# Optimization experiments

Measured on AMD Instinct MI355X. Metric: run time of the kernel, lower is better.

Reference implementation:

```python
import jax, jax.numpy as jnp
import numpy as np

ANG = 5   # angular resolution (u = v = 5, n = 25 views)
CH = 64   # input channels
D = 2 * CH  # spa_dim + ang_dim + fre_dim = c/2 + c/2 + c = 128
NEG = -1e15


def _l2(x):
    # torch F.normalize over the contraction axis (last axis of folded layout)
    n = jnp.sqrt(jnp.sum(x * x, axis=-1, keepdims=True))
    return x / jnp.maximum(n, 1e-12)


def setup_inputs() -> dict:
    key = jax.random.key(0)
    ks = jax.random.split(key, 8)
    b, c, n, h, w = 4, CH, ANG * ANG, 32, 32
    d = D
    return {
        "x_lf": jax.random.normal(ks[0], (b, c, n, h, w), jnp.float32),
        "x_hf": jax.random.normal(ks[1], (b, c, n, h, w), jnp.float32),
        "W_in": jax.random.normal(ks[2], (c, d), jnp.float32) / np.sqrt(c).astype(np.float32),
        "W_kv": jax.random.normal(ks[3], (c, d), jnp.float32) / np.sqrt(c).astype(np.float32),
        "ln_g": jnp.ones((d,), jnp.float32),
        "ln_b": jnp.zeros((d,), jnp.float32),
        "W_m1": jax.random.normal(ks[4], (d, d), jnp.float32) / np.sqrt(d).astype(np.float32),
        "W_m2": jax.random.normal(ks[5], (d, d), jnp.float32) / np.sqrt(d).astype(np.float32),
        "W_out": jax.random.normal(ks[6], (d, c), jnp.float32) / np.sqrt(d).astype(np.float32),
    }


def _attend(fold, unfold, tq, tk, tv):
    # fold(t): (b, cc, u*v, h, w) -> (b, M, K); k/v use the same folding
    qf = _l2(fold(tq))            # q normalized over contraction axis
    kf = _l2(fold(tk))            # k normalized over contraction axis (dim=-2 of k^T)
    vf = fold(tv)
    att = jnp.einsum('bmk,bnk->bmn', qf, kf)   # (b, M, M)
    M = att.shape[-1]
    tril = jnp.tril(jnp.ones((M, M), bool))    # causal mask over folded axis
    att = jax.nn.softmax(jnp.where(tril, att, NEG), axis=-1)
    return unfold(att @ vf) + tv               # residual with token_v


def reference(x_lf, x_hf, W_in, W_kv, ln_g, ln_b, W_m1, W_m2, W_out):
    b, c, n, h, w = x_hf.shape
    u = v = ANG
    d = W_in.shape[1]

    def to_tokens(x, W):
        # 'b c (u v) h w -> (b u v) (h w) c' ; Linear ; back to 'b d (u v) h w'
        xt = x.reshape(b, c, u, v, h, w).transpose(0, 2, 3, 4, 5, 1).reshape(b * u * v, h * w, c)
        y = xt @ W
        return y.reshape(b, u, v, h, w, d).transpose(0, 5, 1, 2, 3, 4).reshape(b, d, u * v, h, w)

    q = to_tokens(x_hf, W_in)
    kv = to_tokens(x_lf, W_kv)
    cq = d // 4
    sf_q, af_q, sa_q = q[:, :cq], q[:, cq:2 * cq], q[:, 2 * cq:]
    sf_kv, af_kv, sa_kv = kv[:, :cq], kv[:, cq:2 * cq], kv[:, 2 * cq:]

    # SpatialFrequency: 'b c (u v) h w -> b (c h) (w u v)'
    def sf_fold(t):
        cc = t.shape[1]
        return t.reshape(b, cc, u, v, h, w).transpose(0, 1, 4, 5, 2, 3).reshape(b, cc * h, w * u * v)
    def sf_unfold(t):
        cc = t.shape[1] // h
        return t.reshape(b, cc, h, w, u, v).transpose(0, 1, 4, 5, 2, 3).reshape(b, cc, u * v, h, w)

    # AngularFrequency: 'b c (u v) h w -> b (c u) (h v w)'
    def af_fold(t):
        cc = t.shape[1]
        return t.reshape(b, cc, u, v, h, w).transpose(0, 1, 2, 4, 3, 5).reshape(b, cc * u, h * v * w)
    def af_unfold(t):
        cc = t.shape[1] // u
        return t.reshape(b, cc, u, h, v, w).transpose(0, 1, 2, 4, 3, 5).reshape(b, cc, u * v, h, w)

    # SpatialAngular: 'b c (u v) h w -> b (h u) (c v w)'
    def sa_fold(t):
        cc = t.shape[1]
        return t.reshape(b, cc, u, v, h, w).transpose(0, 4, 2, 1, 3, 5).reshape(b, h * u, cc * v * w)
    def sa_unfold(t):
        cc = t.shape[2] // (v * w) if t.ndim == 3 else t.shape[1]
        t = t.reshape(b, h, u, cc, v, w)
        return t.transpose(0, 3, 2, 4, 1, 5).reshape(b, cc, u * v, h, w)

    sf = _attend(sf_fold, sf_unfold, sf_q, sf_kv, sf_kv)
    af = _attend(af_fold, af_unfold, af_q, af_kv, af_kv)
    sa = _attend(sa_fold, sa_unfold, sa_q, sa_kv, sa_kv)

    cat = jnp.concatenate([sf, af, sa], axis=1)  # (b, d, n, h, w)
    ct = cat.reshape(b, d, u, v, h, w).transpose(0, 2, 3, 4, 5, 1).reshape(b * u * v, h * w, d)

    # c_mlp: LayerNorm -> Linear -> ReLU -> Linear (dropout is identity in eval)
    mu = jnp.mean(ct, axis=-1, keepdims=True)
    var = jnp.mean(jnp.square(ct - mu), axis=-1, keepdims=True)
    ln = (ct - mu) / jnp.sqrt(var + 1e-5) * ln_g + ln_b
    mlp = jax.nn.relu(ln @ W_m1) @ W_m2
    out_t = (mlp + ct) @ W_out  # residual then output projection

    out = out_t.reshape(b, u, v, h, w, -1).transpose(0, 5, 1, 2, 3, 4).reshape(b, -1, u * v, h, w)
    return out
```

## Files before the change

kernel.cpp:

```cpp
#include <hip/hip_runtime.h>

#define NSP   25600
#define HWC   1024

typedef __attribute__((ext_vector_type(8))) short bf8;
typedef __attribute__((ext_vector_type(4))) float f4;
#define MFMA(a,b,c) __builtin_amdgcn_mfma_f32_16x16x32_bf16(a, b, c, 0, 0, 0)
typedef unsigned short u16;

__device__ __forceinline__ u16 f2b(float f) {
    union { float f; unsigned u; } v; v.f = f;
    unsigned r = v.u + 0x7fffu + ((v.u >> 16) & 1u);
    return (u16)(r >> 16);
}
__device__ __forceinline__ float b2f(u16 h) {
    union { unsigned u; float f; } v; v.u = ((unsigned)h) << 16;
    return v.f;
}

__device__ __forceinline__ long row_base(int att, int b, int m) {
    if (att == 0) { int cc = m >> 5, h = m & 31;   return ((long)(b*128 + cc))*NSP + h*32; }
    else if (att == 1) { int cc = m / 5, u = m - cc*5; return ((long)(b*128 + 32 + cc))*NSP + u*5120; }
    else { int h = m / 5, u = m - h*5;            return ((long)(b*128 + 64))*NSP + u*5120 + h*32; }
}
__device__ __forceinline__ long chunk_off(int att, int kc) {
    if (att == 0) return (long)kc * 1024;
    else if (att == 1) return (long)kc * 32;
    else { int cc = kc / 5, v = kc - cc*5; return (long)cc*NSP + v*1024; }
}

__global__ __launch_bounds__(256) void k_prep(
        const float* __restrict__ Wi, const float* __restrict__ Wk,
        const float* __restrict__ W1, const float* __restrict__ W2,
        const float* __restrict__ Wo, u16* __restrict__ wbt) {
    int e = blockIdx.x * 256 + threadIdx.x;
    const float* src; int base, K, N;
    if (e < 8192)       { src = Wi; base = 0;     K = 64;  N = 128; }
    else if (e < 16384) { src = Wk; base = 8192;  K = 64;  N = 128; }
    else if (e < 32768) { src = W1; base = 16384; K = 128; N = 128; }
    else if (e < 49152) { src = W2; base = 32768; K = 128; N = 128; }
    else                { src = Wo; base = 49152; K = 128; N = 64;  }
    int local = e - base, n = local / K, k = local - n * K;
    wbt[e] = f2b(src[k * N + n]);
}

__global__ __launch_bounds__(256) void k_tokens(
        const float* __restrict__ x_hf, const float* __restrict__ x_lf,
        const u16* __restrict__ wbt,
        u16* __restrict__ qb, u16* __restrict__ kvb) {
    int s0 = blockIdx.x * 64, b = blockIdx.y, which = blockIdx.z;
    const float* x  = which ? x_lf : x_hf;
    const u16* Wb = wbt + (which ? 8192 : 0);
    u16* out = which ? kvb : qb;
    __shared__ u16 Axs[64 * 72];
    __shared__ u16 Wl [128 * 72];
    int tid = threadIdx.x;
    for (int g = tid; g < 1024; g += 256) {
        int d = g >> 3, c8 = (g & 7) * 8;
        *(bf8*)&Wl[d * 72 + c8] = *(const bf8*)(Wb + d * 64 + c8);
    }
    for (int g = tid; g < 1024; g += 256) {
        int s = g & 63, c4 = (g >> 6) * 4;
        long xb = ((long)(b * 64 + c4)) * NSP + s0 + s;
        ushort4 pk;
        pk.x = f2b(x[xb]);
        pk.y = f2b(x[xb + NSP]);
        pk.z = f2b(x[xb + 2 * NSP]);
        pk.w = f2b(x[xb + 3 * NSP]);
        *(ushort4*)&Axs[s * 72 + c4] = pk;
    }
    __syncthreads();
    int w = tid >> 6, l = tid & 63, quad = l >> 4, col = l & 15;
    f4 z = {0.f, 0.f, 0.f, 0.f};
    f4 acc[8]; for (int i = 0; i < 8; ++i) acc[i] = z;
#pragma unroll
    for (int kc = 0; kc < 2; ++kc) {
        bf8 a = *(bf8*)&Axs[(w * 16 + col) * 72 + kc * 32 + quad * 8];
#pragma unroll
        for (int nt = 0; nt < 8; ++nt) {
            bf8 bb = *(bf8*)&Wl[(nt * 16 + col) * 72 + kc * 32 + quad * 8];
            acc[nt] = MFMA(a, bb, acc[nt]);
        }
    }
#pragma unroll
    for (int nt = 0; nt < 8; ++nt) {
        int d = nt * 16 + col;
        long base = ((long)(b * 128 + d)) * NSP + s0 + w * 16 + quad * 4;
        ushort4 pk;
        pk.x = f2b(acc[nt][0]); pk.y = f2b(acc[nt][1]);
        pk.z = f2b(acc[nt][2]); pk.w = f2b(acc[nt][3]);
        *(ushort4*)(out + base) = pk;
    }
}

__global__ __launch_bounds__(256) void k_vt_norms(
        const u16* __restrict__ qb, const u16* __restrict__ kvb,
        u16* __restrict__ vt0, u16* __restrict__ vt1, u16* __restrict__ vt2,
        float* __restrict__ nq, float* __restrict__ nk) {
    int x = blockIdx.x, b = blockIdx.y;
    int tid = threadIdx.x;
    if (x < 3200) {
        int att, kc, pt, P, KC; u16* vt;
        if (x < 800)       { att = 0; kc = x >> 5; pt = (x & 31) * 32; P = 1024; KC = 25;  vt = vt0; }
        else if (x < 1600) { int x2 = x - 800;  att = 1; kc = x2 / 5; pt = (x2 - kc * 5) * 32; P = 160; KC = 160; vt = vt1; }
        else               { int x3 = x - 1600; att = 2; kc = x3 / 5; pt = (x3 - kc * 5) * 32; P = 160; KC = 320; vt = vt2; }
        long co = chunk_off(att, kc);
        __shared__ u16 T[32 * 36];
        {
            int r = tid >> 3, fq = (tid & 7) * 4;
            ushort4 e = *(const ushort4*)(kvb + row_base(att, b, pt + r) + co + fq);
            *(ushort4*)&T[r * 36 + fq] = e;
        }
        __syncthreads();
        {
            int f = tid >> 3, p4 = (tid & 7) * 4;
            ushort4 pk;
            pk.x = T[(p4    ) * 36 + f];
            pk.y = T[(p4 + 1) * 36 + f];
            pk.z = T[(p4 + 2) * 36 + f];
            pk.w = T[(p4 + 3) * 36 + f];
            *(ushort4*)(vt + ((long)b * KC + kc) * 32 * P + (long)f * P + pt + p4) = pk;
        }
    } else {
        int x2 = x - 3200;
        int which = x2 >= 336;
        int g = which ? x2 - 336 : x2;
        int att, m0, KC;
        if (g < 256)      { att = 0; m0 = g * 4;         KC = 25;  }
        else if (g < 296) { att = 1; m0 = (g - 256) * 4; KC = 160; }
        else              { att = 2; m0 = (g - 296) * 4; KC = 320; }
        const u16* src = which ? kvb : qb;
        float* dst = which ? nk : nq;
        int w = tid >> 6, lane = tid & 63;
        int m = m0 + w;
        long base = row_base(att, b, m);
        int K = KC * 32;
        float s = 0.f;
        for (int k8 = lane * 8; k8 < K; k8 += 512) {
            bf8 v = *(const bf8*)(src + base + chunk_off(att, k8 >> 5) + (k8 & 31));
#pragma unroll
            for (int j = 0; j < 8; ++j) { float f = b2f(((u16*)&v)[j]); s += f * f; }
        }
        for (int o = 32; o >= 1; o >>= 1) s += __shfl_xor(s, o);
        if (lane == 0) {
            int off = (att == 0) ? b * 1024 + m
                                 : ((att == 1) ? 4096 : 4736) + b * 160 + m;
            dst[off] = fmaxf(sqrtf(s), 1e-12f);
        }
    }
}

__global__ __launch_bounds__(256) void k_sgemm_all(
        const u16* __restrict__ qb, const u16* __restrict__ kvb,
        const float* __restrict__ nq, const float* __restrict__ nk,
        u16* __restrict__ Sb, float* __restrict__ Spart) {
    __shared__ float lds[4096];
    int x = blockIdx.x, b = blockIdx.y;
    int tid = threadIdx.x, w = tid >> 6, l = tid & 63, quad = l >> 4, col = l & 15;
    if (x < 136) {
        u16* Qs = (u16*)lds;
        u16* Ks = Qs + 64 * 40;
        int t = x, i = 0;
        while (t >= (i + 1) * (i + 2) / 2) ++i;
        int j = t - i * (i + 1) / 2;
        int mt = i * 64, nt = j * 64;
        int srow = tid >> 2, g = tid & 3;
        f4 z = {0.f, 0.f, 0.f, 0.f};
        f4 acc[4]; for (int q = 0; q < 4; ++q) acc[q] = z;
        for (int kc = 0; kc < 25; ++kc) {
            long co = (long)kc * 1024;
            {
                int m = mt + srow;
                *(bf8*)&Qs[srow * 40 + g * 8] =
                    *(const bf8*)(qb + ((long)(b*128 + (m >> 5)))*NSP + (m & 31)*32 + co + g*8);
                int n = nt + srow;
                *(bf8*)&Ks[srow * 40 + g * 8] =
                    *(const bf8*)(kvb + ((long)(b*128 + (n >> 5)))*NSP + (n & 31)*32 + co + g*8);
            }
            __syncthreads();
            bf8 a = *(bf8*)&Qs[(w * 16 + col) * 40 + quad * 8];
#pragma unroll
            for (int t2 = 0; t2 < 4; ++t2) {
                bf8 bb = *(bf8*)&Ks[(t2 * 16 + col) * 40 + quad * 8];
                acc[t2] = MFMA(a, bb, acc[t2]);
            }
            __syncthreads();
        }
#pragma unroll
        for (int t2 = 0; t2 < 4; ++t2)
#pragma unroll
            for (int r = 0; r < 4; ++r) {
                int m = mt + w * 16 + quad * 4 + r, n = nt + t2 * 16 + col;
                float v = (n <= m) ? acc[t2][r] / (nq[b*1024 + m] * nk[b*1024 + n]) : 0.f;
                Sb[((long)b * 1024 + m) * 1024 + n] = f2b(v);
            }
    } else {
        int x2 = x - 136;
        int t = x2 % 15, y = x2 / 15;
        int att, split, nsplit; float* base;
        if (y < 10) { att = 1; split = y;      nsplit = 10; base = Spart; }
        else        { att = 2; split = y - 10; nsplit = 20; base = Spart + 614400; }
        int i = 0;
        while (t >= (i + 1) * (i + 2) / 2) ++i;
        int j = t - i * (i + 1) / 2;
        int mt = i * 32, nt = j * 32;
        long rm0 = row_base(att, b, mt + col),      rm1 = row_base(att, b, mt + 16 + col);
        long rn0 = row_base(att, b, nt + col),      rn1 = row_base(att, b, nt + 16 + col);
        int ko = quad * 8;
        f4 z = {0.f, 0.f, 0.f, 0.f};
        f4 a00 = z, a01 = z, a10 = z, a11 = z;
#pragma unroll
        for (int s = 0; s < 4; ++s) {
            int kc = split * 16 + w * 4 + s;
            long co = chunk_off(att, kc);
            bf8 qa0 = *(const bf8*)(qb + rm0 + co + ko);
            bf8 qa1 = *(const bf8*)(qb + rm1 + co + ko);
            bf8 kb0 = *(const bf8*)(kvb + rn0 + co + ko);
            bf8 kb1 = *(const bf8*)(kvb + rn1 + co + ko);
            a00 = MFMA(qa0, kb0, a00); a01 = MFMA(qa0, kb1, a01);
            a10 = MFMA(qa1, kb0, a10); a11 = MFMA(qa1, kb1, a11);
        }
        float* my = lds + w * 1024;
#pragma unroll
        for (int r = 0; r < 4; ++r) {
            my[(quad * 4 + r) * 32 + col]            = a00[r];
            my[(quad * 4 + r) * 32 + 16 + col]       = a01[r];
            my[(16 + quad * 4 + r) * 32 + col]       = a10[r];
            my[(16 + quad * 4 + r) * 32 + 16 + col]  = a11[r];
        }
        __syncthreads();
        float* dst = base + ((long)((b * 15 + t) * nsplit + split)) * 1024;
        for (int e = tid; e < 1024; e += 256)
            dst[e] = lds[e] + lds[1024 + e] + lds[2048 + e] + lds[3072 + e];
    }
}

__global__ __launch_bounds__(256) void k_softmax_all(
        const u16* __restrict__ Sb, u16* __restrict__ Pb,
        const float* __restrict__ Spart, const float* __restrict__ nq,
        const float* __restrict__ nk, u16* __restrict__ Pb12) {
    int xb = blockIdx.x, b = blockIdx.y, tid = threadIdx.x;
    if (xb < 256) {
        int w = tid >> 6, lane = tid & 63;
        int m = xb * 4 + w;
        const u16* row = Sb + ((long)b * 1024 + m) * 1024;
        u16* pr = Pb + ((long)b * 1024 + m) * 1024;
        int e0 = lane * 16;
        bf8 x0 = *(const bf8*)(row + e0);
        bf8 x1 = *(const bf8*)(row + e0 + 8);
        float v[16];
#pragma unroll
        for (int j = 0; j < 8; ++j) { v[j] = b2f(((u16*)&x0)[j]); v[8 + j] = b2f(((u16*)&x1)[j]); }
        float mx = -1e30f;
#pragma unroll
        for (int j = 0; j < 16; ++j) if (e0 + j <= m) mx = fmaxf(mx, v[j]);
#pragma unroll
        for (int o = 32; o >= 1; o >>= 1) mx = fmaxf(mx, __shfl_xor(mx, o));
        float s = 0.f;
#pragma unroll
        for (int j = 0; j < 16; ++j) {
            float e = (e0 + j <= m) ? __expf(v[j] - mx) : 0.f;
            v[j] = e; s += e;
        }
#pragma unroll
        for (int o = 32; o >= 1; o >>= 1) s += __shfl_xor(s, o);
        float inv = 1.f / s;
        bf8 o0, o1;
#pragma unroll
        for (int j = 0; j < 8; ++j) {
            ((u16*)&o0)[j] = f2b(v[j] * inv);
            ((u16*)&o1)[j] = f2b(v[8 + j] * inv);
        }
        *(bf8*)(pr + e0) = o0;
        *(bf8*)(pr + e0 + 8) = o1;
    } else {
        int x = xb - 256;
        int att = (x < 160) ? 1 : 2;
        int m = (att == 1) ? x : x - 160;
        int nsplit = (att == 1) ? 10 : 20;
        const float* base = (att == 1) ? Spart : Spart + 614400;
        int noff = (att == 1) ? 4096 : 4736;
        u16* P = Pb12 + ((att == 1) ? 0 : 102400);
        int i = m >> 5, ro = (m & 31) * 32;
        int n = tid;
        bool act = (n <= m) && (n < 160);
        float myv = 0.f;
        if (act) {
            int t = i * (i + 1) / 2 + (n >> 5);
            const float* src = base + ((long)((b * 15 + t) * nsplit)) * 1024 + ro + (n & 31);
            float s = 0.f;
            for (int sp = 0; sp < nsplit; ++sp) s += src[(long)sp * 1024];
            myv = s / (nq[noff + b * 160 + m] * nk[noff + b * 160 + n]);
        }
        __shared__ float red[256];
        red[tid] = act ? myv : -1e30f; __syncthreads();
        for (int w = 128; w >= 1; w >>= 1) {
            if (tid < w) red[tid] = fmaxf(red[tid], red[tid + w]);
            __syncthreads();
        }
        float mx = red[0]; __syncthreads();
        float e = act ? __expf(myv - mx) : 0.f;
        red[tid] = e; __syncthreads();
        for (int w = 128; w >= 1; w >>= 1) {
            if (tid < w) red[tid] += red[tid + w];
            __syncthreads();
        }
        float inv = 1.f / red[0];
        if (n < 160) P[((long)b * 160 + m) * 160 + n] = f2b(e * inv);
    }
}

__global__ __launch_bounds__(256) void k_ogemm_all(
        const u16* __restrict__ Pb, const u16* __restrict__ vt0,
        const u16* __restrict__ Pb12, const u16* __restrict__ vt1,
        const u16* __restrict__ vt2, const u16* __restrict__ kvb,
        u16* __restrict__ catb) {
    __shared__ u16 lds[64 * 72 + 32 * 72];
    int x = blockIdx.x, b = blockIdx.y;
    int tid = threadIdx.x, w = tid >> 6, l = tid & 63, quad = l >> 4, col = l & 15;
    if (x < 400) {
        int mtt = x & 15, kc = x >> 4;
        int mt = mtt * 64;
        long co = (long)kc * 1024;
        const u16* vtc = vt0 + ((long)b * 25 + kc) * 32 * 1024;
        u16* Ps = lds;
        u16* Vs = lds + 64 * 72;
        f4 z = {0.f, 0.f, 0.f, 0.f};
        f4 acc[2]; acc[0] = z; acc[1] = z;
        for (int s = 0; s <= mtt; ++s) {
            int p0 = s * 64;
#pragma unroll
            for (int i = 0; i < 2; ++i) {
                int idx = i * 256 + tid;
                int row = idx >> 3, c8 = (idx & 7) * 8;
                *(bf8*)&Ps[row * 72 + c8] =
                    *(const bf8*)(Pb + ((long)(b * 1024 + mt + row)) * 1024 + p0 + c8);
            }
            {
                int f = tid >> 3, p8 = (tid & 7) * 8;
                *(bf8*)&Vs[f * 72 + p8] =
                    *(const bf8*)(vtc + (long)f * 1024 + p0 + p8);
            }
            __syncthreads();
            bf8 a0 = *(bf8*)&Ps[(w * 16 + col) * 72 + quad * 8];
            bf8 a1 = *(bf8*)&Ps[(w * 16 + col) * 72 + 32 + quad * 8];
#pragma unroll
            for (int t2 = 0; t2 < 2; ++t2) {
                bf8 b0 = *(bf8*)&Vs[(t2 * 16 + col) * 72 + quad * 8];
                bf8 b1 = *(bf8*)&Vs[(t2 * 16 + col) * 72 + 32 + quad * 8];
                acc[t2] = MFMA(a0, b0, acc[t2]);
                acc[t2] = MFMA(a1, b1, acc[t2]);
            }
            __syncthreads();
        }
#pragma unroll
        for (int t2 = 0; t2 < 2; ++t2)
#pragma unroll
            for (int r = 0; r < 4; ++r) {
                int m = mt + w * 16 + quad * 4 + r, f = t2 * 16 + col;
                long adr = ((long)(b * 128 + (m >> 5))) * NSP + (m & 31) * 32 + co + f;
                catb[adr] = f2b(acc[t2][r] + b2f(kvb[adr]));
            }
    } else {
        int x2 = x - 400;
        int it = x2 % 5, y = x2 / 5;
        int att, kc, KC; const u16 *vt, *P;
        if (y < 160) { att = 1; kc = y;       KC = 160; vt = vt1; P = Pb12; }
        else         { att = 2; kc = y - 160; KC = 320; vt = vt2; P = Pb12 + 102400; }
        int mt = it * 32;
        const u16* vtc = vt + ((long)b * KC + kc) * 32 * 160;
        u16* Ps = lds;
        u16* Vs = lds + 32 * 40;
        int mh = w & 1, fh = w >> 1;
        f4 acc = {0.f, 0.f, 0.f, 0.f};
        for (int nt2 = 0; nt2 <= it; ++nt2) {
            {
                int row = tid >> 3, g4 = (tid & 7) * 4;
                *(ushort4*)&Ps[row * 40 + g4] =
                    *(const ushort4*)(P + ((long)(b * 160 + mt + row)) * 160 + nt2 * 32 + g4);
                *(ushort4*)&Vs[row * 40 + g4] =
                    *(const ushort4*)(vtc + (long)row * 160 + nt2 * 32 + g4);
            }
            __syncthreads();
            bf8 a  = *(bf8*)&Ps[(mh * 16 + col) * 40 + quad * 8];
            bf8 bb = *(bf8*)&Vs[(fh * 16 + col) * 40 + quad * 8];
            acc = MFMA(a, bb, acc);
            __syncthreads();
        }
#pragma unroll
        for (int r = 0; r < 4; ++r) {
            int m = mt + mh * 16 + quad * 4 + r, f = fh * 16 + col;
            long adr = row_base(att, b, m) + chunk_off(att, kc) + f;
            catb[adr] = f2b(acc[r] + b2f(kvb[adr]));
        }
    }
}

__global__ __launch_bounds__(256) void k_transpose_ln(
        const u16* __restrict__ catb, u16* __restrict__ ctb,
        float* __restrict__ mu, float* __restrict__ rstd) {
    int hwt = blockIdx.x * 16, bn = blockIdx.y;
    int b = bn / 25, uv = bn - b * 25;
    __shared__ u16 T[16 * 136];
    int tid = threadIdx.x;
    const u16* src = catb + (long)b * 128 * NSP + (long)uv * HWC + hwt;
    {
        int d = tid >> 1, hw8 = (tid & 1) * 8;
        bf8 v = *(const bf8*)(src + (long)d * NSP + hw8);
#pragma unroll
        for (int j = 0; j < 8; ++j) T[(hw8 + j) * 136 + d] = ((u16*)&v)[j];
    }
    __syncthreads();
    {
        int w = tid >> 6, l = tid & 63;
        int tk = w * 4 + (l >> 4), dg = (l & 15) * 8;
        bf8 vv = *(bf8*)&T[tk * 136 + dg];
        float s = 0.f, s2 = 0.f;
#pragma unroll
        for (int j = 0; j < 8; ++j) {
            float f = b2f(((u16*)&vv)[j]); s += f; s2 += f * f;
        }
        for (int o = 8; o >= 1; o >>= 1) { s += __shfl_xor(s, o); s2 += __shfl_xor(s2, o); }
        if ((l & 15) == 0) {
            int t = bn * 1024 + hwt + tk;
            float m = s * (1.f / 128.f);
            float var = s2 * (1.f / 128.f) - m * m;
            mu[t] = m; rstd[t] = rsqrtf(var + 1e-5f);
        }
    }
    {
        int hw = tid >> 4, d8 = (tid & 15) * 8;
        *(bf8*)(ctb + ((long)(bn * 1024 + hwt + hw)) * 128 + d8) = *(bf8*)&T[hw * 136 + d8];
    }
}

__global__ __launch_bounds__(256) void k_mlp1(
        const u16* __restrict__ ctb, const float* __restrict__ mu,
        const float* __restrict__ rstd, const float* __restrict__ g,
        const float* __restrict__ be, const u16* __restrict__ wbt,
        u16* __restrict__ h1b) {
    int tt = blockIdx.x * 64, tid = threadIdx.x;
    const u16* W1b = wbt + 16384;
    __shared__ u16 As[64 * 136], Wt[128 * 136];
    __shared__ float gl[128], bl[128];
    if (tid < 128) { gl[tid] = g[tid]; bl[tid] = be[tid]; }
    for (int q = tid; q < 2048; q += 256) {
        int n = q >> 4, k8 = (q & 15) * 8;
        *(bf8*)&Wt[n * 136 + k8] = *(const bf8*)(W1b + n * 128 + k8);
    }
    __syncthreads();
    for (int q = tid; q < 1024; q += 256) {
        int row = q >> 4, k8 = (q & 15) * 8, t = tt + row;
        bf8 cv = *(const bf8*)(ctb + (long)t * 128 + k8);
        float m = mu[t], rs = rstd[t];
        bf8 av;
#pragma unroll
        for (int j = 0; j < 8; ++j)
            ((u16*)&av)[j] = f2b((b2f(((u16*)&cv)[j]) - m) * rs * gl[k8 + j] + bl[k8 + j]);
        *(bf8*)&As[row * 136 + k8] = av;
    }
    __syncthreads();
    int w = tid >> 6, l = tid & 63, quad = l >> 4, col = l & 15;
    f4 z = {0.f, 0.f, 0.f, 0.f};
    f4 acc[8]; for (int i = 0; i < 8; ++i) acc[i] = z;
#pragma unroll
    for (int kc = 0; kc < 4; ++kc) {
        bf8 a = *(bf8*)&As[(w * 16 + col) * 136 + kc * 32 + quad * 8];
#pragma unroll
        for (int nt = 0; nt < 8; ++nt) {
            bf8 bb = *(bf8*)&Wt[(nt * 16 + col) * 136 + kc * 32 + quad * 8];
            acc[nt] = MFMA(a, bb, acc[nt]);
        }
    }
#pragma unroll
    for (int nt = 0; nt < 8; ++nt)
#pragma unroll
        for (int r = 0; r < 4; ++r) {
            int t = tt + w * 16 + quad * 4 + r, n = nt * 16 + col;
            h1b[(long)t * 128 + n] = f2b(fmaxf(acc[nt][r], 0.f));
        }
}

__global__ __launch_bounds__(256) void k_mlp2(
        const u16* __restrict__ h1b, const u16* __restrict__ ctb,
        const u16* __restrict__ wbt, u16* __restrict__ m2b) {
    int tt = blockIdx.x * 64, tid = threadIdx.x;
    const u16* W2b = wbt + 32768;
    __shared__ u16 As[64 * 136], Wt[128 * 136];
    for (int q = tid; q < 2048; q += 256) {
        int n = q >> 4, k8 = (q & 15) * 8;
        *(bf8*)&Wt[n * 136 + k8] = *(const bf8*)(W2b + n * 128 + k8);
    }
    for (int q = tid; q < 1024; q += 256) {
        int row = q >> 4, k8 = (q & 15) * 8;
        *(bf8*)&As[row * 136 + k8] = *(const bf8*)(h1b + (long)(tt + row) * 128 + k8);
    }
    __syncthreads();
    int w = tid >> 6, l = tid & 63, quad = l >> 4, col = l & 15;
    f4 z = {0.f, 0.f, 0.f, 0.f};
    f4 acc[8]; for (int i = 0; i < 8; ++i) acc[i] = z;
#pragma unroll
    for (int kc = 0; kc < 4; ++kc) {
        bf8 a = *(bf8*)&As[(w * 16 + col) * 136 + kc * 32 + quad * 8];
#pragma unroll
        for (int nt = 0; nt < 8; ++nt) {
            bf8 bb = *(bf8*)&Wt[(nt * 16 + col) * 136 + kc * 32 + quad * 8];
            acc[nt] = MFMA(a, bb, acc[nt]);
        }
    }
#pragma unroll
    for (int nt = 0; nt < 8; ++nt)
#pragma unroll
        for (int r = 0; r < 4; ++r) {
            int t = tt + w * 16 + quad * 4 + r, n = nt * 16 + col;
            m2b[(long)t * 128 + n] = f2b(acc[nt][r] + b2f(ctb[(long)t * 128 + n]));
        }
}

__global__ __launch_bounds__(256) void k_out(
        const u16* __restrict__ m2b, const u16* __restrict__ wbt,
        float* __restrict__ out) {
    int tt = blockIdx.x * 64, tid = threadIdx.x;
    const u16* Wob = wbt + 49152;
    __shared__ u16 As[64 * 136], Wt[64 * 136];
    for (int q = tid; q < 1024; q += 256) {
        int o = q >> 4, k8 = (q & 15) * 8;
        *(bf8*)&Wt[o * 136 + k8] = *(const bf8*)(Wob + o * 128 + k8);
    }
    for (int q = tid; q < 1024; q += 256) {
        int row = q >> 4, k8 = (q & 15) * 8;
        *(bf8*)&As[row * 136 + k8] = *(const bf8*)(m2b + (long)(tt + row) * 128 + k8);
    }
    __syncthreads();
    int w = tid >> 6, l = tid & 63, quad = l >> 4, col = l & 15;
    f4 z = {0.f, 0.f, 0.f, 0.f};
    f4 acc[4]; for (int i = 0; i < 4; ++i) acc[i] = z;
#pragma unroll
    for (int kc = 0; kc < 4; ++kc) {
        bf8 a = *(bf8*)&As[(w * 16 + col) * 136 + kc * 32 + quad * 8];
#pragma unroll
        for (int nt = 0; nt < 4; ++nt) {
            bf8 bb = *(bf8*)&Wt[(nt * 16 + col) * 136 + kc * 32 + quad * 8];
            acc[nt] = MFMA(a, bb, acc[nt]);
        }
    }
    int t0 = tt + w * 16 + quad * 4;
    int bn = t0 >> 10, hw = t0 & 1023;
    int b = bn / 25, uv = bn - b * 25;
#pragma unroll
    for (int nt = 0; nt < 4; ++nt) {
        int o = nt * 16 + col;
        float4 pk = {acc[nt][0], acc[nt][1], acc[nt][2], acc[nt][3]};
        *(float4*)(out + ((long)((b * 64 + o) * 25 + uv)) * 1024 + hw) = pk;
    }
}

extern "C" void kernel_launch(void* const* d_in, const int* in_sizes, int n_in,
                              void* d_out, int out_size, void* d_ws, size_t ws_size,
                              hipStream_t stream) {
    const float* x_lf = (const float*)d_in[0];
    const float* x_hf = (const float*)d_in[1];
    const float* W_in = (const float*)d_in[2];
    const float* W_kv = (const float*)d_in[3];
    const float* ln_g = (const float*)d_in[4];
    const float* ln_b = (const float*)d_in[5];
    const float* W_m1 = (const float*)d_in[6];
    const float* W_m2 = (const float*)d_in[7];
    const float* W_ot = (const float*)d_in[8];
    float* out = (float*)d_out;

    float* ws = (float*)d_ws;
    u16*   qb    = (u16*)ws;
    u16*   h1b   = qb;
    u16*   kvb   = (u16*)(ws + 6553600);
    u16*   m2b   = kvb;
    u16*   catb  = (u16*)(ws + 13107200);
    u16*   ctb   = (u16*)(ws + 19660800);
    u16*   Sb    = (u16*)(ws + 26214400);
    u16*   Pb    = (u16*)(ws + 28311552);
    u16*   Pb12  = (u16*)(ws + 30408704);
    float* Spart = ws + 30511104;
    float* nq    = ws + 32354304;
    float* nk    = ws + 32359680;
    float* mu    = ws + 32365056;
    float* rstd  = ws + 32467456;
    u16*   vt0   = (u16*)(ws + 32569856);
    u16*   vt1   = (u16*)(ws + 34208256);
    u16*   vt2   = (u16*)(ws + 35846656);
    u16*   wbt   = (u16*)(ws + 39123456);

    k_prep<<<dim3(224), 256, 0, stream>>>(W_in, W_kv, W_m1, W_m2, W_ot, wbt);

    k_tokens<<<dim3(400, 4, 2), 256, 0, stream>>>(x_hf, x_lf, wbt, qb, kvb);

    k_vt_norms<<<dim3(3872, 4), 256, 0, stream>>>(qb, kvb, vt0, vt1, vt2, nq, nk);

    k_sgemm_all<<<dim3(586, 4), 256, 0, stream>>>(qb, kvb, nq, nk, Sb, Spart);

    k_softmax_all<<<dim3(576, 4), 256, 0, stream>>>(Sb, Pb, Spart, nq, nk, Pb12);

    k_ogemm_all<<<dim3(2800, 4), 256, 0, stream>>>(Pb, vt0, Pb12, vt1, vt2, kvb, catb);

    k_transpose_ln<<<dim3(64, 100), 256, 0, stream>>>(catb, ctb, mu, rstd);

    k_mlp1<<<dim3(1600), 256, 0, stream>>>(ctb, mu, rstd, ln_g, ln_b, wbt, h1b);
    k_mlp2<<<dim3(1600), 256, 0, stream>>>(h1b, ctb, wbt, m2b);
    k_out <<<dim3(1600), 256, 0, stream>>>(m2b, wbt, out);
}
```

Measured before the change: 308.3 us.

## Widen output-GEMM tiles so each block reuses P across many V columns

The P·V output GEMM is retiled. For the first attention, each block now covers 160 feature columns (10 accumulators) instead of 32, so P tiles are loaded far fewer times, and blocks are ordered longest-first. For the other two attentions, each block holds the whole 160x160 P matrix plus a 64-column V slab in LDS and skips the fully masked upper-triangular tiles. The grid drops from 2800 to 320 blocks per batch, which cuts redundant global traffic but increases LDS and register use, lowers occupancy, and may leave parallelism thin.

```diff
diff --git a/kernel.cpp b/kernel.cpp
--- a/kernel.cpp
+++ b/kernel.cpp
@@ -315,84 +315,106 @@
         const u16* __restrict__ Pb12, const u16* __restrict__ vt1,
         const u16* __restrict__ vt2, const u16* __restrict__ kvb,
         u16* __restrict__ catb) {
-    __shared__ u16 lds[64 * 72 + 32 * 72];
+    __shared__ __align__(16) u16 lds[160 * 160 + 64 * 160];
     int x = blockIdx.x, b = blockIdx.y;
     int tid = threadIdx.x, w = tid >> 6, l = tid & 63, quad = l >> 4, col = l & 15;
-    if (x < 400) {
-        int mtt = x & 15, kc = x >> 4;
+    if (x < 80) {
+        int fg = x % 5, mtt = 15 - x / 5;
         int mt = mtt * 64;
-        long co = (long)kc * 1024;
-        const u16* vtc = vt0 + ((long)b * 25 + kc) * 32 * 1024;
         u16* Ps = lds;
         u16* Vs = lds + 64 * 72;
         f4 z = {0.f, 0.f, 0.f, 0.f};
-        f4 acc[2]; acc[0] = z; acc[1] = z;
+        f4 acc[10];
+#pragma unroll
+        for (int i = 0; i < 10; ++i) acc[i] = z;
         for (int s = 0; s <= mtt; ++s) {
             int p0 = s * 64;
 #pragma unroll
             for (int i = 0; i < 2; ++i) {
-                int idx = i * 256 + tid;
-                int row = idx >> 3, c8 = (idx & 7) * 8;
+                int g = i * 256 + tid;
+                int row = g >> 3, c8 = (g & 7) * 8;
                 *(bf8*)&Ps[row * 72 + c8] =
                     *(const bf8*)(Pb + ((long)(b * 1024 + mt + row)) * 1024 + p0 + c8);
             }
-            {
-                int f = tid >> 3, p8 = (tid & 7) * 8;
+#pragma unroll
+            for (int i = 0; i < 5; ++i) {
+                int g = i * 256 + tid;
+                int f = g >> 3, p8 = (g & 7) * 8;
+                int kc = fg * 5 + (f >> 5), fr = f & 31;
                 *(bf8*)&Vs[f * 72 + p8] =
-                    *(const bf8*)(vtc + (long)f * 1024 + p0 + p8);
+                    *(const bf8*)(vt0 + (((long)(b * 25 + kc)) * 32 + fr) * 1024 + p0 + p8);
             }
             __syncthreads();
             bf8 a0 = *(bf8*)&Ps[(w * 16 + col) * 72 + quad * 8];
             bf8 a1 = *(bf8*)&Ps[(w * 16 + col) * 72 + 32 + quad * 8];
 #pragma unroll
-            for (int t2 = 0; t2 < 2; ++t2) {
-                bf8 b0 = *(bf8*)&Vs[(t2 * 16 + col) * 72 + quad * 8];
-                bf8 b1 = *(bf8*)&Vs[(t2 * 16 + col) * 72 + 32 + quad * 8];
-                acc[t2] = MFMA(a0, b0, acc[t2]);
-                acc[t2] = MFMA(a1, b1, acc[t2]);
+            for (int ft = 0; ft < 10; ++ft) {
+                bf8 b0 = *(bf8*)&Vs[(ft * 16 + col) * 72 + quad * 8];
+                bf8 b1 = *(bf8*)&Vs[(ft * 16 + col) * 72 + 32 + quad * 8];
+                acc[ft] = MFMA(a0, b0, acc[ft]);
+                acc[ft] = MFMA(a1, b1, acc[ft]);
             }
             __syncthreads();
         }
 #pragma unroll
-        for (int t2 = 0; t2 < 2; ++t2)
+        for (int ft = 0; ft < 10; ++ft) {
+            int fglob = fg * 160 + ft * 16 + col;
+            int kc = fglob >> 5, fi = fglob & 31;
 #pragma unroll
             for (int r = 0; r < 4; ++r) {
-                int m = mt + w * 16 + quad * 4 + r, f = t2 * 16 + col;
-                long adr = ((long)(b * 128 + (m >> 5))) * NSP + (m & 31) * 32 + co + f;
-                catb[adr] = f2b(acc[t2][r] + b2f(kvb[adr]));
-            }
+                int m = mt + w * 16 + quad * 4 + r;
+                long adr = ((long)(b * 128 + (m >> 5))) * NSP + (m & 31) * 32
+                         + (long)kc * 1024 + fi;
+                catb[adr] = f2b(acc[ft][r] + b2f(kvb[adr]));
+            }
+        }
     } else {
-        int x2 = x - 400;
-        int it = x2 % 5, y = x2 / 5;
-        int att, kc, KC; const u16 *vt, *P;
-        if (y < 160) { att = 1; kc = y;       KC = 160; vt = vt1; P = Pb12; }
-        else         { att = 2; kc = y - 160; KC = 320; vt = vt2; P = Pb12 + 102400; }
-        int mt = it * 32;
-        const u16* vtc = vt + ((long)b * KC + kc) * 32 * 160;
+        int x2 = x - 80;
+        int att = (x2 < 80) ? 1 : 2;
+        int kcg = (att == 1) ? x2 : x2 - 80;
+        int KC  = (att == 1) ? 160 : 320;
+        const u16* vt = (att == 1) ? vt1 : vt2;
+        const u16* P  = Pb12 + ((att == 1) ? 0 : 102400);
         u16* Ps = lds;
-        u16* Vs = lds + 32 * 40;
-        int mh = w & 1, fh = w >> 1;
-        f4 acc = {0.f, 0.f, 0.f, 0.f};
-        for (int nt2 = 0; nt2 <= it; ++nt2) {
-            {
-                int row = tid >> 3, g4 = (tid & 7) * 4;
-                *(ushort4*)&Ps[row * 40 + g4] =
-                    *(const ushort4*)(P + ((long)(b * 160 + mt + row)) * 160 + nt2 * 32 + g4);
-                *(ushort4*)&Vs[row * 40 + g4] =
-                    *(const ushort4*)(vtc + (long)row * 160 + nt2 * 32 + g4);
-            }
-            __syncthreads();
-            bf8 a  = *(bf8*)&Ps[(mh * 16 + col) * 40 + quad * 8];
-            bf8 bb = *(bf8*)&Vs[(fh * 16 + col) * 40 + quad * 8];
-            acc = MFMA(a, bb, acc);
-            __syncthreads();
-        }
-#pragma unroll
-        for (int r = 0; r < 4; ++r) {
-            int m = mt + mh * 16 + quad * 4 + r, f = fh * 16 + col;
-            long adr = row_base(att, b, m) + chunk_off(att, kc) + f;
-            catb[adr] = f2b(acc[r] + b2f(kvb[adr]));
-        }
+        u16* Vs = lds + 160 * 160;
+        for (int g = tid; g < 3200; g += 256) {
+            int row = g / 20, c8 = (g % 20) * 8;
+            *(bf8*)&Ps[row * 160 + c8] =
+                *(const bf8*)(P + ((long)(b * 160 + row)) * 160 + c8);
+        }
+#pragma unroll
+        for (int i = 0; i < 5; ++i) {
+            int g = i * 256 + tid;
+            int f = g / 20, p8 = (g % 20) * 8;
+            int kc = kcg * 2 + (f >> 5), fr = f & 31;
+            *(bf8*)&Vs[f * 160 + p8] =
+                *(const bf8*)(vt + (((long)b * KC + kc) * 32 + fr) * 160 + p8);
+        }
+        __syncthreads();
+        f4 z = {0.f, 0.f, 0.f, 0.f};
+        f4 acc[10];
+#pragma unroll
+        for (int i = 0; i < 10; ++i) acc[i] = z;
+#pragma unroll
+        for (int kk = 0; kk < 5; ++kk) {
+            bf8 bb = *(bf8*)&Vs[(w * 16 + col) * 160 + kk * 32 + quad * 8];
+#pragma unroll
+            for (int mi = 2 * kk; mi < 10; ++mi) {
+                bf8 a = *(bf8*)&Ps[(mi * 16 + col) * 160 + kk * 32 + quad * 8];
+                acc[mi] = MFMA(a, bb, acc[mi]);
+            }
+        }
+        int fglob = kcg * 64 + w * 16 + col;
+        int kc = fglob >> 5, fi = fglob & 31;
+        long cbase = chunk_off(att, kc) + fi;
+#pragma unroll
+        for (int mi = 0; mi < 10; ++mi)
+#pragma unroll
+            for (int r = 0; r < 4; ++r) {
+                int m = mi * 16 + quad * 4 + r;
+                long adr = row_base(att, b, m) + cbase;
+                catb[adr] = f2b(acc[mi][r] + b2f(kvb[adr]));
+            }
     }
 }
 
@@ -599,7 +621,7 @@
 
     k_softmax_all<<<dim3(576, 4), 256, 0, stream>>>(Sb, Pb, Spart, nq, nk, Pb12);
 
-    k_ogemm_all<<<dim3(2800, 4), 256, 0, stream>>>(Pb, vt0, Pb12, vt1, vt2, kvb, catb);
+    k_ogemm_all<<<dim3(320, 4), 256, 0, stream>>>(Pb, vt0, Pb12, vt1, vt2, kvb, catb);
 
     k_transpose_ln<<<dim3(64, 100), 256, 0, stream>>>(catb, ctb, mu, rstd);
 
```

Result: slower. 331.3 us (+7.4%).

## Restructure att1/att2 output GEMM to tile over feature columns with full M per block

Applied to the files above, without the earlier changes.

The angular and spatial-angular P@V branch now gives each block a 16-column feature tile and loops over all 10 row tiles of the 160x160 causal P matrix. The V slice is staged once in LDS, and P is read straight from global memory. Each wave handles up to 3 row tiles and skips the upper causal blocks. This replaces 2400 small blocks with 960, cutting block launch and sync overhead and the repeated V loads, at the cost of uncached P reads and uneven per-wave work.

```diff
diff --git a/kernel.cpp b/kernel.cpp
--- a/kernel.cpp
+++ b/kernel.cpp
@@ -315,7 +315,7 @@
         const u16* __restrict__ Pb12, const u16* __restrict__ vt1,
         const u16* __restrict__ vt2, const u16* __restrict__ kvb,
         u16* __restrict__ catb) {
-    __shared__ u16 lds[64 * 72 + 32 * 72];
+    __shared__ __align__(16) u16 lds[64 * 72 + 32 * 72];
     int x = blockIdx.x, b = blockIdx.y;
     int tid = threadIdx.x, w = tid >> 6, l = tid & 63, quad = l >> 4, col = l & 15;
     if (x < 400) {
@@ -363,35 +363,41 @@
             }
     } else {
         int x2 = x - 400;
-        int it = x2 % 5, y = x2 / 5;
-        int att, kc, KC; const u16 *vt, *P;
-        if (y < 160) { att = 1; kc = y;       KC = 160; vt = vt1; P = Pb12; }
-        else         { att = 2; kc = y - 160; KC = 320; vt = vt2; P = Pb12 + 102400; }
-        int mt = it * 32;
-        const u16* vtc = vt + ((long)b * KC + kc) * 32 * 160;
-        u16* Ps = lds;
-        u16* Vs = lds + 32 * 40;
-        int mh = w & 1, fh = w >> 1;
-        f4 acc = {0.f, 0.f, 0.f, 0.f};
-        for (int nt2 = 0; nt2 <= it; ++nt2) {
-            {
-                int row = tid >> 3, g4 = (tid & 7) * 4;
-                *(ushort4*)&Ps[row * 40 + g4] =
-                    *(const ushort4*)(P + ((long)(b * 160 + mt + row)) * 160 + nt2 * 32 + g4);
-                *(ushort4*)&Vs[row * 40 + g4] =
-                    *(const ushort4*)(vtc + (long)row * 160 + nt2 * 32 + g4);
-            }
-            __syncthreads();
-            bf8 a  = *(bf8*)&Ps[(mh * 16 + col) * 40 + quad * 8];
-            bf8 bb = *(bf8*)&Vs[(fh * 16 + col) * 40 + quad * 8];
-            acc = MFMA(a, bb, acc);
-            __syncthreads();
-        }
-#pragma unroll
-        for (int r = 0; r < 4; ++r) {
-            int m = mt + mh * 16 + quad * 4 + r, f = fh * 16 + col;
-            long adr = row_base(att, b, m) + chunk_off(att, kc) + f;
-            catb[adr] = f2b(acc[r] + b2f(kvb[adr]));
+        int att = (x2 < 320) ? 1 : 2;
+        int ft  = (att == 1) ? x2 : x2 - 320;
+        int KC  = (att == 1) ? 160 : 320;
+        const u16* vt = (att == 1) ? vt1 : vt2;
+        const u16* Prow = Pb12 + ((att == 1) ? 0 : 102400) + (long)b * 160 * 160;
+        u16* Vs = lds;
+        for (int g = tid; g < 320; g += 256) {
+            int fl = g / 20, p8 = (g % 20) * 8;
+            int fglob = ft * 16 + fl;
+            int kc = fglob >> 5, fr = fglob & 31;
+            *(bf8*)&Vs[fl * 168 + p8] =
+                *(const bf8*)(vt + (((long)b * KC + kc) * 32 + fr) * 160 + p8);
+        }
+        __syncthreads();
+        int fglob = ft * 16 + col;
+        int kcf = fglob >> 5, fi = fglob & 31;
+        long cbase = chunk_off(att, kcf) + fi;
+        f4 z = {0.f, 0.f, 0.f, 0.f};
+        for (int j = 0; j < 3; ++j) {
+            int mi = w + 4 * j;
+            if (mi >= 10) break;
+            int nkk = (mi >> 1) + 1;
+            f4 acc = z;
+#pragma unroll 5
+            for (int kk = 0; kk < nkk; ++kk) {
+                bf8 a  = *(const bf8*)(Prow + (mi * 16 + col) * 160 + kk * 32 + quad * 8);
+                bf8 bb = *(bf8*)&Vs[col * 168 + kk * 32 + quad * 8];
+                acc = MFMA(a, bb, acc);
+            }
+#pragma unroll
+            for (int r = 0; r < 4; ++r) {
+                int m = mi * 16 + quad * 4 + r;
+                long adr = row_base(att, b, m) + cbase;
+                catb[adr] = f2b(acc[r] + b2f(kvb[adr]));
+            }
         }
     }
 }
@@ -599,7 +605,7 @@
 
     k_softmax_all<<<dim3(576, 4), 256, 0, stream>>>(Sb, Pb, Spart, nq, nk, Pb12);
 
-    k_ogemm_all<<<dim3(2800, 4), 256, 0, stream>>>(Pb, vt0, Pb12, vt1, vt2, kvb, catb);
+    k_ogemm_all<<<dim3(1360, 4), 256, 0, stream>>>(Pb, vt0, Pb12, vt1, vt2, kvb, catb);
 
     k_transpose_ln<<<dim3(64, 100), 256, 0, stream>>>(catb, ctb, mu, rstd);
 
```

Measured after the change: 310.3 us. No clear change (+0.7%).
